# Optimization experiments

Measured on AMD Instinct MI355X. Metric: run time of the kernel, lower is better.

The kernel has to match this reference:

```python
import jax, jax.numpy as jnp
import numpy as np

EPS_NORM = 1e-12  # F.normalize eps

def _weight_norm(v, g):
    # torch weight_norm with dim=0: W[o,:] = g[o] * v[o,:] / ||v[o,:]||
    return g[:, None] * v / jnp.linalg.norm(v, axis=1, keepdims=True)

def _l2_normalize(x, axis):
    n = jnp.linalg.norm(x, axis=axis, keepdims=True)
    return x / jnp.maximum(n, EPS_NORM)

def setup_inputs() -> dict:
    key = jax.random.key(0)
    ks = jax.random.split(key, 6)
    B, C_emb, T = 16, 1024, 2048
    K, C_cb = 4096, 64
    return {
        "x": jax.random.normal(ks[0], (B, C_emb, T), dtype=jnp.float32),
        "v_in": jax.random.normal(ks[1], (C_cb, C_emb), dtype=jnp.float32) * 0.02,
        "g_in": jax.random.uniform(ks[2], (C_cb,), dtype=jnp.float32, minval=0.5, maxval=1.5),
        "v_out": jax.random.normal(ks[3], (C_emb, C_cb), dtype=jnp.float32) * 0.02,
        "g_out": jax.random.uniform(ks[4], (C_emb,), dtype=jnp.float32, minval=0.5, maxval=1.5),
        "codebook": jax.random.normal(ks[5], (K, C_cb), dtype=jnp.float32),
    }

def reference(x, v_in, g_in, v_out, g_out, codebook):
    sg = jax.lax.stop_gradient
    W_in = _weight_norm(v_in, g_in)    # (C_cb, C_emb)
    W_out = _weight_norm(v_out, g_out)  # (C_emb, C_cb)

    # 1x1 conv projection: (B, C_cb, T)
    x_proj = jnp.einsum('oi,bit->bot', W_in, x)

    # normalize=True: cosine-style nearest neighbor
    emb = _l2_normalize(x_proj, axis=1)           # (B, C_cb, T)
    cb_n = _l2_normalize(codebook, axis=1)        # (K, C_cb)

    e = jnp.swapaxes(emb, 1, 2)                   # (B, T, C_cb)
    # squared euclidean distance (monotone with cdist for argmin)
    dot = jnp.einsum('btc,kc->btk', e, cb_n)      # (B, T, K)
    d2 = (jnp.sum(e * e, axis=-1, keepdims=True)
          - 2.0 * dot
          + jnp.sum(cb_n * cb_n, axis=-1))
    codes = jnp.argmin(d2, axis=-1)               # (B, T) int

    # gather from the UN-normalized codebook (matches torch code)
    quantized_e = codebook[codes]                 # (B, T, C_cb)
    q = jnp.swapaxes(quantized_e, 1, 2)           # (B, C_cb, T)

    codebook_loss = jnp.mean((sg(x_proj) - q) ** 2)
    commit_loss = jnp.mean((x_proj - sg(q)) ** 2)

    quantized_proj = x_proj + sg(q - x_proj)      # straight-through
    quantized = jnp.einsum('oc,bct->bot', W_out, quantized_proj)  # (B, C_emb, T)

    return codes, quantized, codebook_loss, commit_loss, x_proj, quantized_proj
```

## Files before the change

kernel.cpp:

```cpp
#include <hip/hip_runtime.h>
#include <math.h>

#define BB 16
#define CE 1024
#define TT 2048
#define KK 4096
#define CC 64

#define O_CODES 0
#define O_QUANT 32768
#define O_CBL   33587200
#define O_CML   33587201
#define O_XPROJ 33587202
#define O_QPROJ 35684354

#define W_WINF  0
#define W_WOUTF 262144
#define W_CBSQ  327680
#define W_NORMS 331776
#define W_CODES 364544
#define W_PB    397312
#define W_PIDX  528384
#define W_LOSS  659456
#define W_BF    659520

typedef __attribute__((ext_vector_type(8))) _Float16 half8;
typedef __attribute__((ext_vector_type(4))) float f32x4;

__global__ __launch_bounds__(64) void prep_kernel(
    const float* __restrict__ v_in, const float* __restrict__ g_in,
    const float* __restrict__ v_out, const float* __restrict__ g_out,
    const float* __restrict__ cb, float* __restrict__ ws) {
  int bid = blockIdx.x, tid = threadIdx.x;
  if (bid == 0 && tid == 0) ws[W_LOSS] = 0.f;
  if (bid < 64) {
    int o = bid;
    float s = 0.f;
    for (int i = tid; i < CE; i += 64) { float v = v_in[o * CE + i]; s += v * v; }
    for (int off = 32; off; off >>= 1) s += __shfl_down(s, off);
    s = __shfl(s, 0);
    float norm = sqrtf(s);
    float g = g_in[o];
    _Float16* wf = (_Float16*)(ws + W_WINF);
    int ot = o >> 4, m = o & 15;
    for (int i = tid; i < CE; i += 64) {
      float w = (g * v_in[o * CE + i]) / norm;
      _Float16 hi = (_Float16)w;
      _Float16 lo = (_Float16)(w - (float)hi);
      int ks = i >> 5, q = (i >> 3) & 3, j = i & 7;
      int lane = q * 16 + m;
      int base = ((ot * 32 + ks) * 64 + lane) * 8 + j;
      wf[base] = hi;
      wf[65536 + base] = lo;
    }
  } else if (bid < 64 + CE) {
    int o = bid - 64;
    int c = tid;
    float v = v_out[o * CC + c];
    float s = v * v;
    for (int off = 32; off; off >>= 1) s += __shfl_down(s, off);
    s = __shfl(s, 0);
    float w = (g_out[o] * v) / sqrtf(s);
    _Float16 hi = (_Float16)w;
    _Float16 lo = (_Float16)(w - (float)hi);
    _Float16* wf = (_Float16*)(ws + W_WOUTF);
    int ot = o >> 4, m = o & 15;
    int ks = c >> 5, q = (c >> 3) & 3, j = c & 7;
    int lane = q * 16 + m;
    int base = ((ot * 2 + ks) * 64 + lane) * 8 + j;
    wf[base] = hi;
    wf[131072 / 2 + base] = lo;
  } else {
    int k = bid - 64 - CE;
    int c = tid;
    float v = cb[k * CC + c];
    float s = v * v;
    for (int off = 32; off; off >>= 1) s += __shfl_down(s, off);
    s = __shfl(s, 0);
    float n = fmaxf(sqrtf(s), 1e-12f);
    float cn = v / n;
    float s2 = cn * cn;
    for (int off = 32; off; off >>= 1) s2 += __shfl_down(s2, off);
    if (tid == 0) ws[W_CBSQ + k] = s2;
    _Float16 hi = (_Float16)cn;
    _Float16 lo = (_Float16)(cn - (float)hi);
    _Float16* bfh = (_Float16*)(ws + W_BF);
    int ntile = k >> 4, ki = c >> 5;
    int lane = ((c >> 3) & 3) * 16 + (k & 15);
    int j = c & 7;
    int idx = (((ntile * 2 + ki) * 64 + lane) << 3) + j;
    bfh[idx] = hi;
    bfh[262144 + idx] = lo;
  }
}

__global__ __launch_bounds__(256) void proj_in_kernel(
    const float* __restrict__ x, const half8* __restrict__ wf,
    float* __restrict__ out, float* __restrict__ norms) {
  int tid = threadIdx.x;
  int w = tid >> 6, l = tid & 63;
  int n = l & 15, q = l >> 4;
  int blk = blockIdx.x;
  int b = blk >> 5, t0 = (blk & 31) * 64;
  int t = t0 + w * 16 + n;
  const float* xp = x + (size_t)b * CE * TT + t;

  f32x4 acc[4];
#pragma unroll
  for (int ot = 0; ot < 4; ++ot) acc[ot] = (f32x4){0.f, 0.f, 0.f, 0.f};

  for (int ks = 0; ks < 32; ++ks) {
    int kb = ks * 32 + q * 8;
    float v[8];
#pragma unroll
    for (int j = 0; j < 8; ++j) v[j] = xp[(size_t)(kb + j) * TT];
    half8 xh, xl;
#pragma unroll
    for (int j = 0; j < 8; ++j) xh[j] = (_Float16)v[j];
#pragma unroll
    for (int j = 0; j < 8; ++j) xl[j] = (_Float16)(v[j] - (float)xh[j]);
    half8 wh[4], wl[4];
#pragma unroll
    for (int ot = 0; ot < 4; ++ot) {
      wh[ot] = wf[(ot * 32 + ks) * 64 + l];
      wl[ot] = wf[8192 + (ot * 32 + ks) * 64 + l];
    }
#pragma unroll
    for (int ot = 0; ot < 4; ++ot)
      acc[ot] = __builtin_amdgcn_mfma_f32_16x16x32_f16(wh[ot], xh, acc[ot], 0, 0, 0);
#pragma unroll
    for (int ot = 0; ot < 4; ++ot)
      acc[ot] = __builtin_amdgcn_mfma_f32_16x16x32_f16(wh[ot], xl, acc[ot], 0, 0, 0);
#pragma unroll
    for (int ot = 0; ot < 4; ++ot)
      acc[ot] = __builtin_amdgcn_mfma_f32_16x16x32_f16(wl[ot], xh, acc[ot], 0, 0, 0);
  }

  float s = 0.f;
#pragma unroll
  for (int ot = 0; ot < 4; ++ot) {
#pragma unroll
    for (int r = 0; r < 4; ++r) {
      float vv = acc[ot][r];
      out[O_XPROJ + (size_t)(b * CC + ot * 16 + q * 4 + r) * TT + t] = vv;
      s = fmaf(vv, vv, s);
    }
  }
  s += __shfl_xor(s, 16);
  s += __shfl_xor(s, 32);
  if (q == 0) norms[b * TT + t] = fmaxf(sqrtf(s), 1e-12f);
}

__global__ __launch_bounds__(256) void dist_kernel(
    const float* __restrict__ xproj, const float* __restrict__ norms,
    const float* __restrict__ cbsq, const uint4* __restrict__ bf,
    float* __restrict__ pbest, int* __restrict__ pidx) {
  __shared__ uint4 ldsB[2048];
  int tid = threadIdx.x;
  int l = tid & 63, w = tid >> 6;
  int blk = blockIdx.x;
  int tb = blk >> 2, ks = blk & 3;
  int b = tb >> 3, t0 = (tb & 7) * 256;
  int m = l & 15, q = l >> 4;

  half8 Ahi[4][2], Alo[4][2];
  const float* xpB = xproj + (size_t)b * CC * TT;
#pragma unroll
  for (int bd = 0; bd < 4; ++bd) {
    int t = t0 + w * 64 + bd * 16 + m;
    float n = norms[b * TT + t];
#pragma unroll
    for (int ki = 0; ki < 2; ++ki) {
      int cbase = ki * 32 + q * 8;
#pragma unroll
      for (int j = 0; j < 8; ++j) {
        float v = xpB[(cbase + j) * TT + t] / n;
        _Float16 h = (_Float16)v;
        Ahi[bd][ki][j] = h;
        Alo[bd][ki][j] = (_Float16)(v - (float)h);
      }
    }
  }

  float best[4][4];
  int bidx[4][4];
#pragma unroll
  for (int bd = 0; bd < 4; ++bd)
#pragma unroll
    for (int r = 0; r < 4; ++r) { best[bd][r] = 3.4e38f; bidx[bd][r] = 0; }

  for (int cc = 0; cc < 8; ++cc) {
    int nt0 = ks * 64 + cc * 8;
    __syncthreads();
#pragma unroll
    for (int r = 0; r < 4; ++r) {
      int u = r * 256 + tid;
      ldsB[u] = bf[nt0 * 128 + u];
      ldsB[1024 + u] = bf[32768 + nt0 * 128 + u];
    }
    __syncthreads();
#pragma unroll
    for (int ntl = 0; ntl < 8; ++ntl) {
      int kbase = (nt0 + ntl) * 16;
      float cq = cbsq[kbase + m];
      half8 Bhi0 = *(const half8*)&ldsB[ntl * 128 + l];
      half8 Bhi1 = *(const half8*)&ldsB[ntl * 128 + 64 + l];
      half8 Blo0 = *(const half8*)&ldsB[1024 + ntl * 128 + l];
      half8 Blo1 = *(const half8*)&ldsB[1024 + ntl * 128 + 64 + l];
      f32x4 acc[4];
#pragma unroll
      for (int bd = 0; bd < 4; ++bd) acc[bd] = (f32x4){0.f, 0.f, 0.f, 0.f};
#pragma unroll
      for (int bd = 0; bd < 4; ++bd)
        acc[bd] = __builtin_amdgcn_mfma_f32_16x16x32_f16(Ahi[bd][0], Bhi0, acc[bd], 0, 0, 0);
#pragma unroll
      for (int bd = 0; bd < 4; ++bd)
        acc[bd] = __builtin_amdgcn_mfma_f32_16x16x32_f16(Ahi[bd][1], Bhi1, acc[bd], 0, 0, 0);
#pragma unroll
      for (int bd = 0; bd < 4; ++bd)
        acc[bd] = __builtin_amdgcn_mfma_f32_16x16x32_f16(Alo[bd][0], Bhi0, acc[bd], 0, 0, 0);
#pragma unroll
      for (int bd = 0; bd < 4; ++bd)
        acc[bd] = __builtin_amdgcn_mfma_f32_16x16x32_f16(Alo[bd][1], Bhi1, acc[bd], 0, 0, 0);
#pragma unroll
      for (int bd = 0; bd < 4; ++bd)
        acc[bd] = __builtin_amdgcn_mfma_f32_16x16x32_f16(Ahi[bd][0], Blo0, acc[bd], 0, 0, 0);
#pragma unroll
      for (int bd = 0; bd < 4; ++bd)
        acc[bd] = __builtin_amdgcn_mfma_f32_16x16x32_f16(Ahi[bd][1], Blo1, acc[bd], 0, 0, 0);
      int kl = kbase + m;
#pragma unroll
      for (int bd = 0; bd < 4; ++bd)
#pragma unroll
        for (int r = 0; r < 4; ++r) {
          float sc = fmaf(-2.f, acc[bd][r], cq);
          if (sc < best[bd][r]) { best[bd][r] = sc; bidx[bd][r] = kl; }
        }
    }
  }

#pragma unroll
  for (int st = 1; st < 16; st <<= 1) {
#pragma unroll
    for (int bd = 0; bd < 4; ++bd)
#pragma unroll
      for (int r = 0; r < 4; ++r) {
        float os = __shfl_xor(best[bd][r], st);
        int oi = __shfl_xor(bidx[bd][r], st);
        if (os < best[bd][r] || (os == best[bd][r] && oi < bidx[bd][r])) {
          best[bd][r] = os;
          bidx[bd][r] = oi;
        }
      }
  }
  if (m == 0) {
#pragma unroll
    for (int bd = 0; bd < 4; ++bd)
#pragma unroll
      for (int r = 0; r < 4; ++r) {
        int t = t0 + w * 64 + bd * 16 + q * 4 + r;
        int gt = b * TT + t;
        pbest[ks * 32768 + gt] = best[bd][r];
        pidx[ks * 32768 + gt] = bidx[bd][r];
      }
  }
}

__global__ __launch_bounds__(256) void merge_kernel(
    const float* __restrict__ pbest, const int* __restrict__ pidx,
    float* __restrict__ out, int* __restrict__ codes_i) {
  int gt = blockIdx.x * 256 + threadIdx.x;
  float bs = pbest[gt];
  int bi = pidx[gt];
#pragma unroll
  for (int s = 1; s < 4; ++s) {
    float s2 = pbest[s * 32768 + gt];
    int i2 = pidx[s * 32768 + gt];
    if (s2 < bs || (s2 == bs && i2 < bi)) { bs = s2; bi = i2; }
  }
  out[O_CODES + gt] = (float)bi;
  codes_i[gt] = bi;
}

__global__ __launch_bounds__(256) void gather_kernel(
    const float* __restrict__ cb, const half8* __restrict__ wf,
    const int* __restrict__ codes_i, float* __restrict__ out,
    float* __restrict__ loss_acc) {
  int tid = threadIdx.x;
  int w = tid >> 6, l = tid & 63;
  int n = l & 15, q = l >> 4;
  int blk = blockIdx.x;
  int b = blk >> 5, t0 = (blk & 31) * 64;
  int t = t0 + w * 16 + n;

  int code = codes_i[b * TT + t];
  const float* cbr = cb + (size_t)code * CC;
  float qv[2][8];
#pragma unroll
  for (int ks = 0; ks < 2; ++ks) {
    float4 a = *(const float4*)&cbr[ks * 32 + q * 8];
    float4 c4 = *(const float4*)&cbr[ks * 32 + q * 8 + 4];
    qv[ks][0] = a.x; qv[ks][1] = a.y; qv[ks][2] = a.z; qv[ks][3] = a.w;
    qv[ks][4] = c4.x; qv[ks][5] = c4.y; qv[ks][6] = c4.z; qv[ks][7] = c4.w;
  }

  float ls = 0.f;
#pragma unroll
  for (int ks = 0; ks < 2; ++ks)
#pragma unroll
    for (int j = 0; j < 8; ++j) {
      int c = ks * 32 + q * 8 + j;
      size_t g = (size_t)(b * CC + c) * TT + t;
      float qq = qv[ks][j];
      out[O_QPROJ + g] = qq;
      float d = out[O_XPROJ + g] - qq;
      ls = fmaf(d, d, ls);
    }
  for (int off = 32; off; off >>= 1) ls += __shfl_down(ls, off);
  if (l == 0) atomicAdd(loss_acc, ls);

  half8 qh[2], ql[2];
#pragma unroll
  for (int ks = 0; ks < 2; ++ks) {
#pragma unroll
    for (int j = 0; j < 8; ++j) {
      qh[ks][j] = (_Float16)qv[ks][j];
      ql[ks][j] = (_Float16)(qv[ks][j] - (float)qh[ks][j]);
    }
  }

  for (int ot = 0; ot < 64; ++ot) {
    half8 wh0 = wf[(ot * 2 + 0) * 64 + l];
    half8 wh1 = wf[(ot * 2 + 1) * 64 + l];
    half8 wl0 = wf[8192 + (ot * 2 + 0) * 64 + l];
    half8 wl1 = wf[8192 + (ot * 2 + 1) * 64 + l];
    f32x4 acc = (f32x4){0.f, 0.f, 0.f, 0.f};
    acc = __builtin_amdgcn_mfma_f32_16x16x32_f16(wh0, qh[0], acc, 0, 0, 0);
    acc = __builtin_amdgcn_mfma_f32_16x16x32_f16(wh1, qh[1], acc, 0, 0, 0);
    acc = __builtin_amdgcn_mfma_f32_16x16x32_f16(wh0, ql[0], acc, 0, 0, 0);
    acc = __builtin_amdgcn_mfma_f32_16x16x32_f16(wh1, ql[1], acc, 0, 0, 0);
    acc = __builtin_amdgcn_mfma_f32_16x16x32_f16(wl0, qh[0], acc, 0, 0, 0);
    acc = __builtin_amdgcn_mfma_f32_16x16x32_f16(wl1, qh[1], acc, 0, 0, 0);
#pragma unroll
    for (int r = 0; r < 4; ++r)
      out[O_QUANT + (size_t)(b * CE + ot * 16 + q * 4 + r) * TT + t] = acc[r];
  }
}

__global__ void finalize_kernel(const float* __restrict__ ws, float* __restrict__ out) {
  if (threadIdx.x == 0 && blockIdx.x == 0) {
    float l = ws[W_LOSS] / 2097152.f;
    out[O_CBL] = l;
    out[O_CML] = l;
  }
}

extern "C" void kernel_launch(void* const* d_in, const int* in_sizes, int n_in,
                              void* d_out, int out_size, void* d_ws, size_t ws_size,
                              hipStream_t stream) {
  const float* x     = (const float*)d_in[0];
  const float* v_in  = (const float*)d_in[1];
  const float* g_in  = (const float*)d_in[2];
  const float* v_out = (const float*)d_in[3];
  const float* g_out = (const float*)d_in[4];
  const float* cb    = (const float*)d_in[5];
  float* out = (float*)d_out;
  float* ws  = (float*)d_ws;
  int* codes_i = (int*)(ws + W_CODES);

  prep_kernel<<<64 + 1024 + 4096, 64, 0, stream>>>(v_in, g_in, v_out, g_out, cb, ws);
  proj_in_kernel<<<512, 256, 0, stream>>>(x, (const half8*)(ws + W_WINF),
                                          out, ws + W_NORMS);
  dist_kernel<<<512, 256, 0, stream>>>(out + O_XPROJ, ws + W_NORMS,
                                       ws + W_CBSQ, (const uint4*)(ws + W_BF),
                                       ws + W_PB, (int*)(ws + W_PIDX));
  merge_kernel<<<128, 256, 0, stream>>>(ws + W_PB, (const int*)(ws + W_PIDX),
                                        out, codes_i);
  gather_kernel<<<512, 256, 0, stream>>>(cb, (const half8*)(ws + W_WOUTF),
                                         codes_i, out, ws + W_LOSS);
  finalize_kernel<<<1, 64, 0, stream>>>(ws, out);
}
```

Before: 402.1 us.

## Fuse projection, distance argmin, merge and gather into one kernel

Replaces the four kernels for projection, distance, merge and gather/output projection with a single fused kernel per 64-timestep block. x_proj and norms stay in LDS, and the four waves each scan a quarter of the codebook, with the argmin merged through shared memory. Weight and codebook fragments are now register double-buffered straight from global memory instead of staged through LDS. This removes intermediate global round-trips and launch gaps. In exchange, each block now holds all 64 timesteps across the whole codebook scan with higher register pressure, so fewer blocks may be resident.

```diff
diff --git a/kernel.cpp b/kernel.cpp
--- a/kernel.cpp
+++ b/kernel.cpp
@@ -17,10 +17,6 @@
 #define W_WINF  0
 #define W_WOUTF 262144
 #define W_CBSQ  327680
-#define W_NORMS 331776
-#define W_CODES 364544
-#define W_PB    397312
-#define W_PIDX  528384
 #define W_LOSS  659456
 #define W_BF    659520
 
@@ -94,256 +90,273 @@
   }
 }
 
-__global__ __launch_bounds__(256) void proj_in_kernel(
-    const float* __restrict__ x, const half8* __restrict__ wf,
-    float* __restrict__ out, float* __restrict__ norms) {
+__global__ __launch_bounds__(256, 2) void fused_kernel(
+    const float* __restrict__ x, const float* __restrict__ cb,
+    const float* __restrict__ ws, float* __restrict__ out,
+    float* loss_acc) {
+  __shared__ float xls[64][68];
+  __shared__ float nrmS[64];
+  __shared__ float pbS[4][64];
+  __shared__ int   piS[4][64];
+  __shared__ int   codeS[64];
+
   int tid = threadIdx.x;
   int w = tid >> 6, l = tid & 63;
   int n = l & 15, q = l >> 4;
   int blk = blockIdx.x;
   int b = blk >> 5, t0 = (blk & 31) * 64;
-  int t = t0 + w * 16 + n;
-  const float* xp = x + (size_t)b * CE * TT + t;
-
-  f32x4 acc[4];
-#pragma unroll
-  for (int ot = 0; ot < 4; ++ot) acc[ot] = (f32x4){0.f, 0.f, 0.f, 0.f};
-
-  for (int ks = 0; ks < 32; ++ks) {
-    int kb = ks * 32 + q * 8;
-    float v[8];
-#pragma unroll
-    for (int j = 0; j < 8; ++j) v[j] = xp[(size_t)(kb + j) * TT];
-    half8 xh, xl;
-#pragma unroll
-    for (int j = 0; j < 8; ++j) xh[j] = (_Float16)v[j];
-#pragma unroll
-    for (int j = 0; j < 8; ++j) xl[j] = (_Float16)(v[j] - (float)xh[j]);
-    half8 wh[4], wl[4];
+
+  const half8* wfin = (const half8*)(ws + W_WINF);
+  const half8* wfo  = (const half8*)(ws + W_WOUTF);
+  const half8* bfr  = (const half8*)(ws + W_BF);
+  const float* cbsq = ws + W_CBSQ;
+
+  {
+    int t = t0 + w * 16 + n;
+    const float* xp = x + (size_t)b * CE * TT + t;
+    f32x4 acc[4];
+#pragma unroll
+    for (int ot = 0; ot < 4; ++ot) acc[ot] = (f32x4){0.f, 0.f, 0.f, 0.f};
+
+    float v[2][8];
+    half8 wh[2][4], wl[2][4];
+#pragma unroll
+    for (int j = 0; j < 8; ++j) v[0][j] = xp[(size_t)(q * 8 + j) * TT];
 #pragma unroll
     for (int ot = 0; ot < 4; ++ot) {
-      wh[ot] = wf[(ot * 32 + ks) * 64 + l];
-      wl[ot] = wf[8192 + (ot * 32 + ks) * 64 + l];
-    }
-#pragma unroll
-    for (int ot = 0; ot < 4; ++ot)
-      acc[ot] = __builtin_amdgcn_mfma_f32_16x16x32_f16(wh[ot], xh, acc[ot], 0, 0, 0);
-#pragma unroll
-    for (int ot = 0; ot < 4; ++ot)
-      acc[ot] = __builtin_amdgcn_mfma_f32_16x16x32_f16(wh[ot], xl, acc[ot], 0, 0, 0);
-#pragma unroll
-    for (int ot = 0; ot < 4; ++ot)
-      acc[ot] = __builtin_amdgcn_mfma_f32_16x16x32_f16(wl[ot], xh, acc[ot], 0, 0, 0);
-  }
-
-  float s = 0.f;
-#pragma unroll
-  for (int ot = 0; ot < 4; ++ot) {
-#pragma unroll
-    for (int r = 0; r < 4; ++r) {
-      float vv = acc[ot][r];
-      out[O_XPROJ + (size_t)(b * CC + ot * 16 + q * 4 + r) * TT + t] = vv;
-      s = fmaf(vv, vv, s);
-    }
-  }
-  s += __shfl_xor(s, 16);
-  s += __shfl_xor(s, 32);
-  if (q == 0) norms[b * TT + t] = fmaxf(sqrtf(s), 1e-12f);
-}
-
-__global__ __launch_bounds__(256) void dist_kernel(
-    const float* __restrict__ xproj, const float* __restrict__ norms,
-    const float* __restrict__ cbsq, const uint4* __restrict__ bf,
-    float* __restrict__ pbest, int* __restrict__ pidx) {
-  __shared__ uint4 ldsB[2048];
-  int tid = threadIdx.x;
-  int l = tid & 63, w = tid >> 6;
-  int blk = blockIdx.x;
-  int tb = blk >> 2, ks = blk & 3;
-  int b = tb >> 3, t0 = (tb & 7) * 256;
-  int m = l & 15, q = l >> 4;
-
-  half8 Ahi[4][2], Alo[4][2];
-  const float* xpB = xproj + (size_t)b * CC * TT;
-#pragma unroll
-  for (int bd = 0; bd < 4; ++bd) {
-    int t = t0 + w * 64 + bd * 16 + m;
-    float n = norms[b * TT + t];
-#pragma unroll
-    for (int ki = 0; ki < 2; ++ki) {
-      int cbase = ki * 32 + q * 8;
+      wh[0][ot] = wfin[(ot * 32 + 0) * 64 + l];
+      wl[0][ot] = wfin[8192 + (ot * 32 + 0) * 64 + l];
+    }
+#pragma unroll 2
+    for (int ks = 0; ks < 32; ++ks) {
+      int cur = ks & 1;
+      if (ks < 31) {
+        int kb = (ks + 1) * 32 + q * 8;
+#pragma unroll
+        for (int j = 0; j < 8; ++j) v[cur ^ 1][j] = xp[(size_t)(kb + j) * TT];
+#pragma unroll
+        for (int ot = 0; ot < 4; ++ot) {
+          wh[cur ^ 1][ot] = wfin[(ot * 32 + ks + 1) * 64 + l];
+          wl[cur ^ 1][ot] = wfin[8192 + (ot * 32 + ks + 1) * 64 + l];
+        }
+      }
+      half8 xh, xl;
+#pragma unroll
+      for (int j = 0; j < 8; ++j) xh[j] = (_Float16)v[cur][j];
+#pragma unroll
+      for (int j = 0; j < 8; ++j) xl[j] = (_Float16)(v[cur][j] - (float)xh[j]);
+#pragma unroll
+      for (int ot = 0; ot < 4; ++ot)
+        acc[ot] = __builtin_amdgcn_mfma_f32_16x16x32_f16(wh[cur][ot], xh, acc[ot], 0, 0, 0);
+#pragma unroll
+      for (int ot = 0; ot < 4; ++ot)
+        acc[ot] = __builtin_amdgcn_mfma_f32_16x16x32_f16(wh[cur][ot], xl, acc[ot], 0, 0, 0);
+#pragma unroll
+      for (int ot = 0; ot < 4; ++ot)
+        acc[ot] = __builtin_amdgcn_mfma_f32_16x16x32_f16(wl[cur][ot], xh, acc[ot], 0, 0, 0);
+    }
+
+    float s = 0.f;
+    int tl = w * 16 + n;
+#pragma unroll
+    for (int ot = 0; ot < 4; ++ot) {
+#pragma unroll
+      for (int r = 0; r < 4; ++r) {
+        float vv = acc[ot][r];
+        out[O_XPROJ + (size_t)(b * CC + ot * 16 + q * 4 + r) * TT + t] = vv;
+        s = fmaf(vv, vv, s);
+      }
+      *(f32x4*)&xls[tl][ot * 16 + q * 4] = acc[ot];
+    }
+    s += __shfl_xor(s, 16);
+    s += __shfl_xor(s, 32);
+    if (l < 16) nrmS[tl] = fmaxf(sqrtf(s), 1e-12f);
+  }
+  __syncthreads();
+
+  {
+    half8 Ahi[4][2], Alo[4][2];
+#pragma unroll
+    for (int bd = 0; bd < 4; ++bd) {
+      int tl = bd * 16 + n;
+      float nv = nrmS[tl];
+#pragma unroll
+      for (int ki = 0; ki < 2; ++ki) {
+#pragma unroll
+        for (int j = 0; j < 8; ++j) {
+          float vv = xls[tl][ki * 32 + q * 8 + j] / nv;
+          _Float16 h = (_Float16)vv;
+          Ahi[bd][ki][j] = h;
+          Alo[bd][ki][j] = (_Float16)(vv - (float)h);
+        }
+      }
+    }
+
+    float best[4][4];
+    int bidx[4][4];
+#pragma unroll
+    for (int bd = 0; bd < 4; ++bd)
+#pragma unroll
+      for (int r = 0; r < 4; ++r) { best[bd][r] = 3.4e38f; bidx[bd][r] = 0; }
+
+    half8 Bh0[2], Bh1[2], Bl0[2], Bl1[2];
+    float cq[2];
+    {
+      int nt = w * 64;
+      Bh0[0] = bfr[(nt * 2 + 0) * 64 + l];
+      Bh1[0] = bfr[(nt * 2 + 1) * 64 + l];
+      Bl0[0] = bfr[32768 + (nt * 2 + 0) * 64 + l];
+      Bl1[0] = bfr[32768 + (nt * 2 + 1) * 64 + l];
+      cq[0] = cbsq[nt * 16 + n];
+    }
+#pragma unroll 2
+    for (int it = 0; it < 64; ++it) {
+      int cur = it & 1;
+      int nt = w * 64 + it;
+      if (it < 63) {
+        int nt2 = nt + 1;
+        Bh0[cur ^ 1] = bfr[(nt2 * 2 + 0) * 64 + l];
+        Bh1[cur ^ 1] = bfr[(nt2 * 2 + 1) * 64 + l];
+        Bl0[cur ^ 1] = bfr[32768 + (nt2 * 2 + 0) * 64 + l];
+        Bl1[cur ^ 1] = bfr[32768 + (nt2 * 2 + 1) * 64 + l];
+        cq[cur ^ 1] = cbsq[nt2 * 16 + n];
+      }
+      f32x4 acc[4];
+#pragma unroll
+      for (int bd = 0; bd < 4; ++bd) acc[bd] = (f32x4){0.f, 0.f, 0.f, 0.f};
+#pragma unroll
+      for (int bd = 0; bd < 4; ++bd)
+        acc[bd] = __builtin_amdgcn_mfma_f32_16x16x32_f16(Ahi[bd][0], Bh0[cur], acc[bd], 0, 0, 0);
+#pragma unroll
+      for (int bd = 0; bd < 4; ++bd)
+        acc[bd] = __builtin_amdgcn_mfma_f32_16x16x32_f16(Ahi[bd][1], Bh1[cur], acc[bd], 0, 0, 0);
+#pragma unroll
+      for (int bd = 0; bd < 4; ++bd)
+        acc[bd] = __builtin_amdgcn_mfma_f32_16x16x32_f16(Alo[bd][0], Bh0[cur], acc[bd], 0, 0, 0);
+#pragma unroll
+      for (int bd = 0; bd < 4; ++bd)
+        acc[bd] = __builtin_amdgcn_mfma_f32_16x16x32_f16(Alo[bd][1], Bh1[cur], acc[bd], 0, 0, 0);
+#pragma unroll
+      for (int bd = 0; bd < 4; ++bd)
+        acc[bd] = __builtin_amdgcn_mfma_f32_16x16x32_f16(Ahi[bd][0], Bl0[cur], acc[bd], 0, 0, 0);
+#pragma unroll
+      for (int bd = 0; bd < 4; ++bd)
+        acc[bd] = __builtin_amdgcn_mfma_f32_16x16x32_f16(Ahi[bd][1], Bl1[cur], acc[bd], 0, 0, 0);
+
+      int kl = nt * 16 + n;
+#pragma unroll
+      for (int bd = 0; bd < 4; ++bd)
+#pragma unroll
+        for (int r = 0; r < 4; ++r) {
+          float sc = fmaf(-2.f, acc[bd][r], cq[cur]);
+          if (sc < best[bd][r]) { best[bd][r] = sc; bidx[bd][r] = kl; }
+        }
+    }
+
+#pragma unroll
+    for (int st = 1; st < 16; st <<= 1) {
+#pragma unroll
+      for (int bd = 0; bd < 4; ++bd)
+#pragma unroll
+        for (int r = 0; r < 4; ++r) {
+          float os = __shfl_xor(best[bd][r], st);
+          int oi = __shfl_xor(bidx[bd][r], st);
+          if (os < best[bd][r] || (os == best[bd][r] && oi < bidx[bd][r])) {
+            best[bd][r] = os;
+            bidx[bd][r] = oi;
+          }
+        }
+    }
+    if (n == 0) {
+#pragma unroll
+      for (int bd = 0; bd < 4; ++bd)
+#pragma unroll
+        for (int r = 0; r < 4; ++r) {
+          int tl = bd * 16 + q * 4 + r;
+          pbS[w][tl] = best[bd][r];
+          piS[w][tl] = bidx[bd][r];
+        }
+    }
+  }
+  __syncthreads();
+
+  if (tid < 64) {
+    float bs = pbS[0][tid];
+    int bi = piS[0][tid];
+#pragma unroll
+    for (int s = 1; s < 4; ++s) {
+      float s2 = pbS[s][tid];
+      int i2 = piS[s][tid];
+      if (s2 < bs || (s2 == bs && i2 < bi)) { bs = s2; bi = i2; }
+    }
+    codeS[tid] = bi;
+    out[O_CODES + b * TT + t0 + tid] = (float)bi;
+  }
+  __syncthreads();
+
+  {
+    int t = t0 + w * 16 + n;
+    int tl = w * 16 + n;
+    int code = codeS[tl];
+    const float* cbr = cb + (size_t)code * CC;
+    float qv[2][8];
+#pragma unroll
+    for (int ks = 0; ks < 2; ++ks) {
+      float4 a = *(const float4*)&cbr[ks * 32 + q * 8];
+      float4 c4 = *(const float4*)&cbr[ks * 32 + q * 8 + 4];
+      qv[ks][0] = a.x; qv[ks][1] = a.y; qv[ks][2] = a.z; qv[ks][3] = a.w;
+      qv[ks][4] = c4.x; qv[ks][5] = c4.y; qv[ks][6] = c4.z; qv[ks][7] = c4.w;
+    }
+
+    float ls = 0.f;
+#pragma unroll
+    for (int ks = 0; ks < 2; ++ks)
 #pragma unroll
       for (int j = 0; j < 8; ++j) {
-        float v = xpB[(cbase + j) * TT + t] / n;
-        _Float16 h = (_Float16)v;
-        Ahi[bd][ki][j] = h;
-        Alo[bd][ki][j] = (_Float16)(v - (float)h);
-      }
-    }
-  }
-
-  float best[4][4];
-  int bidx[4][4];
-#pragma unroll
-  for (int bd = 0; bd < 4; ++bd)
-#pragma unroll
-    for (int r = 0; r < 4; ++r) { best[bd][r] = 3.4e38f; bidx[bd][r] = 0; }
-
-  for (int cc = 0; cc < 8; ++cc) {
-    int nt0 = ks * 64 + cc * 8;
-    __syncthreads();
-#pragma unroll
-    for (int r = 0; r < 4; ++r) {
-      int u = r * 256 + tid;
-      ldsB[u] = bf[nt0 * 128 + u];
-      ldsB[1024 + u] = bf[32768 + nt0 * 128 + u];
-    }
-    __syncthreads();
-#pragma unroll
-    for (int ntl = 0; ntl < 8; ++ntl) {
-      int kbase = (nt0 + ntl) * 16;
-      float cq = cbsq[kbase + m];
-      half8 Bhi0 = *(const half8*)&ldsB[ntl * 128 + l];
-      half8 Bhi1 = *(const half8*)&ldsB[ntl * 128 + 64 + l];
-      half8 Blo0 = *(const half8*)&ldsB[1024 + ntl * 128 + l];
-      half8 Blo1 = *(const half8*)&ldsB[1024 + ntl * 128 + 64 + l];
-      f32x4 acc[4];
-#pragma unroll
-      for (int bd = 0; bd < 4; ++bd) acc[bd] = (f32x4){0.f, 0.f, 0.f, 0.f};
-#pragma unroll
-      for (int bd = 0; bd < 4; ++bd)
-        acc[bd] = __builtin_amdgcn_mfma_f32_16x16x32_f16(Ahi[bd][0], Bhi0, acc[bd], 0, 0, 0);
-#pragma unroll
-      for (int bd = 0; bd < 4; ++bd)
-        acc[bd] = __builtin_amdgcn_mfma_f32_16x16x32_f16(Ahi[bd][1], Bhi1, acc[bd], 0, 0, 0);
-#pragma unroll
-      for (int bd = 0; bd < 4; ++bd)
-        acc[bd] = __builtin_amdgcn_mfma_f32_16x16x32_f16(Alo[bd][0], Bhi0, acc[bd], 0, 0, 0);
-#pragma unroll
-      for (int bd = 0; bd < 4; ++bd)
-        acc[bd] = __builtin_amdgcn_mfma_f32_16x16x32_f16(Alo[bd][1], Bhi1, acc[bd], 0, 0, 0);
-#pragma unroll
-      for (int bd = 0; bd < 4; ++bd)
-        acc[bd] = __builtin_amdgcn_mfma_f32_16x16x32_f16(Ahi[bd][0], Blo0, acc[bd], 0, 0, 0);
-#pragma unroll
-      for (int bd = 0; bd < 4; ++bd)
-        acc[bd] = __builtin_amdgcn_mfma_f32_16x16x32_f16(Ahi[bd][1], Blo1, acc[bd], 0, 0, 0);
-      int kl = kbase + m;
-#pragma unroll
-      for (int bd = 0; bd < 4; ++bd)
-#pragma unroll
-        for (int r = 0; r < 4; ++r) {
-          float sc = fmaf(-2.f, acc[bd][r], cq);
-          if (sc < best[bd][r]) { best[bd][r] = sc; bidx[bd][r] = kl; }
-        }
-    }
-  }
-
-#pragma unroll
-  for (int st = 1; st < 16; st <<= 1) {
-#pragma unroll
-    for (int bd = 0; bd < 4; ++bd)
-#pragma unroll
-      for (int r = 0; r < 4; ++r) {
-        float os = __shfl_xor(best[bd][r], st);
-        int oi = __shfl_xor(bidx[bd][r], st);
-        if (os < best[bd][r] || (os == best[bd][r] && oi < bidx[bd][r])) {
-          best[bd][r] = os;
-          bidx[bd][r] = oi;
-        }
-      }
-  }
-  if (m == 0) {
-#pragma unroll
-    for (int bd = 0; bd < 4; ++bd)
-#pragma unroll
-      for (int r = 0; r < 4; ++r) {
-        int t = t0 + w * 64 + bd * 16 + q * 4 + r;
-        int gt = b * TT + t;
-        pbest[ks * 32768 + gt] = best[bd][r];
-        pidx[ks * 32768 + gt] = bidx[bd][r];
-      }
-  }
-}
-
-__global__ __launch_bounds__(256) void merge_kernel(
-    const float* __restrict__ pbest, const int* __restrict__ pidx,
-    float* __restrict__ out, int* __restrict__ codes_i) {
-  int gt = blockIdx.x * 256 + threadIdx.x;
-  float bs = pbest[gt];
-  int bi = pidx[gt];
-#pragma unroll
-  for (int s = 1; s < 4; ++s) {
-    float s2 = pbest[s * 32768 + gt];
-    int i2 = pidx[s * 32768 + gt];
-    if (s2 < bs || (s2 == bs && i2 < bi)) { bs = s2; bi = i2; }
-  }
-  out[O_CODES + gt] = (float)bi;
-  codes_i[gt] = bi;
-}
-
-__global__ __launch_bounds__(256) void gather_kernel(
-    const float* __restrict__ cb, const half8* __restrict__ wf,
-    const int* __restrict__ codes_i, float* __restrict__ out,
-    float* __restrict__ loss_acc) {
-  int tid = threadIdx.x;
-  int w = tid >> 6, l = tid & 63;
-  int n = l & 15, q = l >> 4;
-  int blk = blockIdx.x;
-  int b = blk >> 5, t0 = (blk & 31) * 64;
-  int t = t0 + w * 16 + n;
-
-  int code = codes_i[b * TT + t];
-  const float* cbr = cb + (size_t)code * CC;
-  float qv[2][8];
-#pragma unroll
-  for (int ks = 0; ks < 2; ++ks) {
-    float4 a = *(const float4*)&cbr[ks * 32 + q * 8];
-    float4 c4 = *(const float4*)&cbr[ks * 32 + q * 8 + 4];
-    qv[ks][0] = a.x; qv[ks][1] = a.y; qv[ks][2] = a.z; qv[ks][3] = a.w;
-    qv[ks][4] = c4.x; qv[ks][5] = c4.y; qv[ks][6] = c4.z; qv[ks][7] = c4.w;
-  }
-
-  float ls = 0.f;
-#pragma unroll
-  for (int ks = 0; ks < 2; ++ks)
-#pragma unroll
-    for (int j = 0; j < 8; ++j) {
-      int c = ks * 32 + q * 8 + j;
-      size_t g = (size_t)(b * CC + c) * TT + t;
-      float qq = qv[ks][j];
-      out[O_QPROJ + g] = qq;
-      float d = out[O_XPROJ + g] - qq;
-      ls = fmaf(d, d, ls);
-    }
-  for (int off = 32; off; off >>= 1) ls += __shfl_down(ls, off);
-  if (l == 0) atomicAdd(loss_acc, ls);
-
-  half8 qh[2], ql[2];
-#pragma unroll
-  for (int ks = 0; ks < 2; ++ks) {
-#pragma unroll
-    for (int j = 0; j < 8; ++j) {
-      qh[ks][j] = (_Float16)qv[ks][j];
-      ql[ks][j] = (_Float16)(qv[ks][j] - (float)qh[ks][j]);
-    }
-  }
-
-  for (int ot = 0; ot < 64; ++ot) {
-    half8 wh0 = wf[(ot * 2 + 0) * 64 + l];
-    half8 wh1 = wf[(ot * 2 + 1) * 64 + l];
-    half8 wl0 = wf[8192 + (ot * 2 + 0) * 64 + l];
-    half8 wl1 = wf[8192 + (ot * 2 + 1) * 64 + l];
-    f32x4 acc = (f32x4){0.f, 0.f, 0.f, 0.f};
-    acc = __builtin_amdgcn_mfma_f32_16x16x32_f16(wh0, qh[0], acc, 0, 0, 0);
-    acc = __builtin_amdgcn_mfma_f32_16x16x32_f16(wh1, qh[1], acc, 0, 0, 0);
-    acc = __builtin_amdgcn_mfma_f32_16x16x32_f16(wh0, ql[0], acc, 0, 0, 0);
-    acc = __builtin_amdgcn_mfma_f32_16x16x32_f16(wh1, ql[1], acc, 0, 0, 0);
-    acc = __builtin_amdgcn_mfma_f32_16x16x32_f16(wl0, qh[0], acc, 0, 0, 0);
-    acc = __builtin_amdgcn_mfma_f32_16x16x32_f16(wl1, qh[1], acc, 0, 0, 0);
-#pragma unroll
-    for (int r = 0; r < 4; ++r)
-      out[O_QUANT + (size_t)(b * CE + ot * 16 + q * 4 + r) * TT + t] = acc[r];
+        int c = ks * 32 + q * 8 + j;
+        float qq = qv[ks][j];
+        out[O_QPROJ + (size_t)(b * CC + c) * TT + t] = qq;
+        float d = xls[tl][c] - qq;
+        ls = fmaf(d, d, ls);
+      }
+    for (int off = 32; off; off >>= 1) ls += __shfl_down(ls, off);
+    if (l == 0) atomicAdd(loss_acc, ls);
+
+    half8 qh[2], ql[2];
+#pragma unroll
+    for (int ks = 0; ks < 2; ++ks)
+#pragma unroll
+      for (int j = 0; j < 8; ++j) {
+        qh[ks][j] = (_Float16)qv[ks][j];
+        ql[ks][j] = (_Float16)(qv[ks][j] - (float)qh[ks][j]);
+      }
+
+    half8 wc[2][4];
+    wc[0][0] = wfo[0 * 64 + l];
+    wc[0][1] = wfo[1 * 64 + l];
+    wc[0][2] = wfo[8192 + 0 * 64 + l];
+    wc[0][3] = wfo[8192 + 1 * 64 + l];
+#pragma unroll 2
+    for (int ot = 0; ot < 64; ++ot) {
+      int cur = ot & 1;
+      if (ot < 63) {
+        int o2 = ot + 1;
+        wc[cur ^ 1][0] = wfo[(o2 * 2 + 0) * 64 + l];
+        wc[cur ^ 1][1] = wfo[(o2 * 2 + 1) * 64 + l];
+        wc[cur ^ 1][2] = wfo[8192 + (o2 * 2 + 0) * 64 + l];
+        wc[cur ^ 1][3] = wfo[8192 + (o2 * 2 + 1) * 64 + l];
+      }
+      f32x4 acc = (f32x4){0.f, 0.f, 0.f, 0.f};
+      acc = __builtin_amdgcn_mfma_f32_16x16x32_f16(wc[cur][0], qh[0], acc, 0, 0, 0);
+      acc = __builtin_amdgcn_mfma_f32_16x16x32_f16(wc[cur][1], qh[1], acc, 0, 0, 0);
+      acc = __builtin_amdgcn_mfma_f32_16x16x32_f16(wc[cur][0], ql[0], acc, 0, 0, 0);
+      acc = __builtin_amdgcn_mfma_f32_16x16x32_f16(wc[cur][1], ql[1], acc, 0, 0, 0);
+      acc = __builtin_amdgcn_mfma_f32_16x16x32_f16(wc[cur][2], qh[0], acc, 0, 0, 0);
+      acc = __builtin_amdgcn_mfma_f32_16x16x32_f16(wc[cur][3], qh[1], acc, 0, 0, 0);
+#pragma unroll
+      for (int r = 0; r < 4; ++r)
+        out[O_QUANT + (size_t)(b * CE + ot * 16 + q * 4 + r) * TT + t] = acc[r];
+    }
   }
 }
 
@@ -366,17 +379,8 @@
   const float* cb    = (const float*)d_in[5];
   float* out = (float*)d_out;
   float* ws  = (float*)d_ws;
-  int* codes_i = (int*)(ws + W_CODES);
 
   prep_kernel<<<64 + 1024 + 4096, 64, 0, stream>>>(v_in, g_in, v_out, g_out, cb, ws);
-  proj_in_kernel<<<512, 256, 0, stream>>>(x, (const half8*)(ws + W_WINF),
-                                          out, ws + W_NORMS);
-  dist_kernel<<<512, 256, 0, stream>>>(out + O_XPROJ, ws + W_NORMS,
-                                       ws + W_CBSQ, (const uint4*)(ws + W_BF),
-                                       ws + W_PB, (int*)(ws + W_PIDX));
-  merge_kernel<<<128, 256, 0, stream>>>(ws + W_PB, (const int*)(ws + W_PIDX),
-                                        out, codes_i);
-  gather_kernel<<<512, 256, 0, stream>>>(cb, (const half8*)(ws + W_WOUTF),
-                                         codes_i, out, ws + W_LOSS);
+  fused_kernel<<<512, 256, 0, stream>>>(x, cb, ws, out, ws + W_LOSS);
   finalize_kernel<<<1, 64, 0, stream>>>(ws, out);
 }
```

Result: faster. 346.9 us (-13.7%).
